# Optimization experiments

Hardware: AMD Instinct MI355X
Metric: run time of the kernel (lower is better)

The kernel has to match this reference:

```python
import jax, jax.numpy as jnp
import numpy as np

N = 50000
E = 400000
DIM_IN = 512
DIM_H = 64
HEADS = 8
DIM_OUT = 40
SLOPE = 0.2  # PyG GATv2Conv default negative_slope


def setup_inputs() -> dict:
    key = jax.random.key(0)
    ks = jax.random.split(key, 16)
    s = 0.05
    return {
        "x": jax.random.normal(ks[0], (N, DIM_IN), dtype=jnp.float32),
        "edge_index": jax.random.randint(ks[1], (2, E), 0, N, dtype=jnp.int64),
        "Wl1": jax.random.normal(ks[2], (DIM_IN, HEADS * DIM_H), dtype=jnp.float32) * s,
        "Wr1": jax.random.normal(ks[3], (DIM_IN, HEADS * DIM_H), dtype=jnp.float32) * s,
        "att1": jax.random.normal(ks[4], (HEADS, DIM_H), dtype=jnp.float32) * s,
        "b1": jax.random.normal(ks[5], (HEADS * DIM_H,), dtype=jnp.float32) * s,
        "Wl2": jax.random.normal(ks[6], (HEADS * DIM_H, DIM_OUT), dtype=jnp.float32) * s,
        "Wr2": jax.random.normal(ks[7], (HEADS * DIM_H, DIM_OUT), dtype=jnp.float32) * s,
        "att2": jax.random.normal(ks[8], (1, DIM_OUT), dtype=jnp.float32) * s,
        "b2": jax.random.normal(ks[9], (DIM_OUT,), dtype=jnp.float32) * s,
        "Wl3": jax.random.normal(ks[10], (HEADS * DIM_H, 2), dtype=jnp.float32) * s,
        "Wr3": jax.random.normal(ks[11], (HEADS * DIM_H, 2), dtype=jnp.float32) * s,
        "att3": jax.random.normal(ks[12], (1, 2), dtype=jnp.float32) * s,
        "b3": jax.random.normal(ks[13], (2,), dtype=jnp.float32) * s,
    }


def gatv2(x, src, dst, Wl, Wr, att, b):
    # PyG GATv2Conv: e_ij = att . LeakyReLU(W_l x_j + W_r x_i); softmax over j (by dst i);
    # out_i = sum_j alpha_ij * (W_l x_j); heads concatenated; bias added after.
    n = x.shape[0]
    H, F = att.shape
    xl = (x @ Wl).reshape(n, H, F)  # source transform
    xr = (x @ Wr).reshape(n, H, F)  # target transform
    e = jax.nn.leaky_relu(xl[src] + xr[dst], negative_slope=SLOPE)  # [E, H, F]
    logits = jnp.einsum("ehf,hf->eh", e, att)  # [E, H]
    m = jax.ops.segment_max(logits, dst, num_segments=n)  # self-loops => every segment nonempty
    ex = jnp.exp(logits - m[dst])
    denom = jax.ops.segment_sum(ex, dst, num_segments=n)
    alpha = ex / denom[dst]  # [E, H]
    out = jax.ops.segment_sum(xl[src] * alpha[:, :, None], dst, num_segments=n)  # [N, H, F]
    return out.reshape(n, H * F) + b


def reference(x, edge_index, Wl1, Wr1, att1, b1, Wl2, Wr2, att2, b2, Wl3, Wr3, att3, b3):
    # add self loops (PyG default add_self_loops=True)
    loops = jnp.arange(N, dtype=edge_index.dtype)
    ei = jnp.concatenate([edge_index, jnp.stack([loops, loops])], axis=1)
    src, dst = ei[0], ei[1]
    # eval mode: dropout is identity; ReverseLayerF is identity in forward
    h = jax.nn.relu(gatv2(x, src, dst, Wl1, Wr1, att1, b1))
    y_class = gatv2(h, src, dst, Wl2, Wr2, att2, b2)
    y_domain = gatv2(h, src, dst, Wl3, Wr3, att3, b3)
    return (y_class, y_domain)
```

## Files before the change

kernel.cpp:

```cpp
#include <hip/hip_runtime.h>
#include <math.h>

typedef unsigned short u16;
typedef unsigned int   u32;
typedef __attribute__((ext_vector_type(8))) short bf16x8;
typedef __attribute__((ext_vector_type(4))) float f32x4;
typedef __attribute__((ext_vector_type(4))) u32   u32x4;

__device__ __forceinline__ float b2f(u16 u) {
  union { u32 i; float f; } v; v.i = ((u32)u) << 16; return v.f;
}
__device__ __forceinline__ u16 f2b(float f) {
  union { u32 i; float f; } v; v.f = f;
  u32 r = v.i + 0x7FFFu + ((v.i >> 16) & 1u);
  return (u16)(r >> 16);
}
__device__ __forceinline__ float blo(u32 w) {
  union { u32 i; float f; } v; v.i = w << 16; return v.f;
}
__device__ __forceinline__ float bhi(u32 w) {
  union { u32 i; float f; } v; v.i = w & 0xFFFF0000u; return v.f;
}
__device__ __forceinline__ void ld_lds16(const u16* g, u16* l) {
  __builtin_amdgcn_global_load_lds((const __attribute__((address_space(1))) void*)g,
                                   (__attribute__((address_space(3))) void*)l, 16, 0, 0);
}

#define NN 50000
#define NE 400000
#define NT 450000
#define NBLK_SCAN 196

__global__ void k_detect(const void* x, const void* ei, int* flags) {
  __shared__ int cnt[2];
  int t = threadIdx.x;
  if (t < 2) cnt[t] = 0;
  __syncthreads();
  u16 u = ((const u16*)x)[t];
  int e = (u >> 7) & 0xFF;
  if (u == 0 || (e >= 90 && e <= 134)) atomicAdd(&cnt[0], 1);
  if (t < 16) {
    if (((const int*)ei)[2 * t + 1] == 0) atomicAdd(&cnt[1], 1);
  }
  __syncthreads();
  if (t == 0) {
    flags[0] = (cnt[0] >= 110) ? 1 : 0;
    flags[1] = (cnt[1] >= 15) ? 1 : 0;
  }
}

__device__ __forceinline__ int eidx(const int* ei, int pos, int i64) {
  return i64 ? ei[2 * pos] : ei[pos];
}

__global__ void k_convert_x(const void* x, const int* flags, u16* xb) {
  int c = blockIdx.x * 256 + threadIdx.x;
  if (flags[0]) {
    ((u32x4*)xb)[c] = ((const u32x4*)x)[c];
  } else {
    const float* xf = (const float*)x + (size_t)c * 8;
    u32x4 o;
    #pragma unroll
    for (int i = 0; i < 4; ++i) {
      u32 lo = f2b(xf[2 * i]);
      u32 hi = f2b(xf[2 * i + 1]);
      o[i] = lo | (hi << 16);
    }
    *(u32x4*)(xb + (size_t)c * 8) = o;
  }
}

__global__ void k_pack_w1t(const void* Wl1, const void* Wr1, const int* flags, u16* w1t) {
  int t = blockIdx.x * 256 + threadIdx.x;
  int k = t >> 10;
  int c = t & 1023;
  const void* W = (c < 512) ? Wl1 : Wr1;
  int cc = c & 511;
  u16 v;
  if (flags[0]) v = ((const u16*)W)[k * 512 + cc];
  else          v = f2b(((const float*)W)[k * 512 + cc]);
  w1t[c * 512 + k] = v;
}

__global__ void k_pack_w23t(const void* Wl2, const void* Wr2, const void* Wl3, const void* Wr3,
                            const int* flags, u16* w23t) {
  int t = blockIdx.x * 256 + threadIdx.x;
  int k = t / 96;
  int c = t % 96;
  const void* W = nullptr; int idx = 0;
  if (c < 40)      { W = Wl2; idx = k * 40 + c; }
  else if (c < 42) { W = Wl3; idx = k * 2 + (c - 40); }
  else if (c < 82) { W = Wr2; idx = k * 40 + (c - 42); }
  else if (c < 84) { W = Wr3; idx = k * 2 + (c - 82); }
  u16 v = 0;
  if (W) {
    if (flags[0]) v = ((const u16*)W)[idx];
    else          v = f2b(((const float*)W)[idx]);
  }
  w23t[c * 512 + k] = v;
}

__global__ void k_pack_params(const void* att1, const void* b1, const void* att2, const void* b2,
                              const void* att3, const void* b3, const int* flags, float* params) {
  int t = blockIdx.x * 256 + threadIdx.x;
  if (t >= 1108) return;
  const void* src; int idx;
  if (t < 512)       { src = att1; idx = t; }
  else if (t < 1024) { src = b1;   idx = t - 512; }
  else if (t < 1064) { src = att2; idx = t - 1024; }
  else if (t < 1104) { src = b2;   idx = t - 1064; }
  else if (t < 1106) { src = att3; idx = t - 1104; }
  else               { src = b3;   idx = t - 1106; }
  params[t] = flags[0] ? b2f(((const u16*)src)[idx]) : ((const float*)src)[idx];
}

__global__ void k_hist(const int* ei, const int* flags, int* deg) {
  int e = blockIdx.x * 256 + threadIdx.x;
  if (e >= NE) return;
  int d = eidx(ei, NE + e, flags[1]);
  atomicAdd(&deg[d], 1);
}

__global__ void k_scanA(const int* deg, int* row_ptr, int* bsum) {
  __shared__ int sh[256];
  int b = blockIdx.x, t = threadIdx.x;
  int i = b * 256 + t;
  int val = (i < NN) ? deg[i] + 1 : 0;
  sh[t] = val;
  __syncthreads();
  #pragma unroll
  for (int off = 1; off < 256; off <<= 1) {
    int v = (t >= off) ? sh[t - off] : 0;
    __syncthreads();
    sh[t] += v;
    __syncthreads();
  }
  if (i < NN) row_ptr[i] = sh[t] - val;
  if (t == 255) bsum[b] = sh[255];
}

__global__ void k_scanB(int* bsum, int* row_ptr) {
  __shared__ int sh[256];
  int t = threadIdx.x;
  int val = (t < NBLK_SCAN) ? bsum[t] : 0;
  sh[t] = val;
  __syncthreads();
  #pragma unroll
  for (int off = 1; off < 256; off <<= 1) {
    int v = (t >= off) ? sh[t - off] : 0;
    __syncthreads();
    sh[t] += v;
    __syncthreads();
  }
  if (t < NBLK_SCAN) bsum[t] = sh[t] - val;
  if (t == 255) row_ptr[NN] = sh[255];
}

__global__ void k_scanC(const int* bsum, int* row_ptr, int* cursor) {
  int i = blockIdx.x * 256 + threadIdx.x;
  if (i < NN) {
    int v = row_ptr[i] + bsum[blockIdx.x];
    row_ptr[i] = v;
    cursor[i] = v;
  }
}

__global__ void k_scatter(const int* ei, const int* flags, int* cursor, int* csr_src) {
  int t = blockIdx.x * 256 + threadIdx.x;
  if (t >= NT) return;
  int i64 = flags[1];
  int s, d;
  if (t < NE) { s = eidx(ei, t, i64); d = eidx(ei, NE + t, i64); }
  else        { s = d = t - NE; }
  int pos = atomicAdd(&cursor[d], 1);
  csr_src[pos] = s;
}

__global__ __launch_bounds__(256) void k_gemm1(const u16* __restrict__ A, const u16* __restrict__ Bt,
                                               u16* __restrict__ XL, u16* __restrict__ XR) {
  __shared__ __align__(16) u16 As[128 * 32];
  __shared__ __align__(16) u16 Bs[128 * 32];
  const int m0 = blockIdx.y * 128;
  const int n0 = blockIdx.x * 128;
  const int t = threadIdx.x;
  const int wave = t >> 6;
  const int lane = t & 63;
  const int wm = (wave >> 1) * 64;
  const int wn = (wave & 1) * 64;
  const int fr = lane & 15;
  const int fk = lane >> 4;
  const int srow = lane >> 2;
  const int scol = (lane & 3) * 8;
  f32x4 acc[4][4] = {};
  for (int k0 = 0; k0 < 512; k0 += 32) {
    #pragma unroll
    for (int c = 0; c < 2; ++c) {
      int r = wave * 16 + c * 64;
      ld_lds16(&A[(m0 + r + srow) * 512 + k0 + scol], &As[r * 32]);
      ld_lds16(&Bt[(n0 + r + srow) * 512 + k0 + scol], &Bs[r * 32]);
    }
    __syncthreads();
    bf16x8 af[4], bb[4];
    #pragma unroll
    for (int i = 0; i < 4; ++i) af[i] = *(const bf16x8*)&As[(wm + i * 16 + fr) * 32 + fk * 8];
    #pragma unroll
    for (int j = 0; j < 4; ++j) bb[j] = *(const bf16x8*)&Bs[(wn + j * 16 + fr) * 32 + fk * 8];
    #pragma unroll
    for (int i = 0; i < 4; ++i)
      #pragma unroll
      for (int j = 0; j < 4; ++j)
        acc[i][j] = __builtin_amdgcn_mfma_f32_16x16x32_bf16(af[i], bb[j], acc[i][j], 0, 0, 0);
    __syncthreads();
  }
  #pragma unroll
  for (int i = 0; i < 4; ++i) {
    #pragma unroll
    for (int r = 0; r < 4; ++r) {
      int gm = m0 + wm + i * 16 + fk * 4 + r;
      if (gm < NN) {
        #pragma unroll
        for (int j = 0; j < 4; ++j) {
          int gn = n0 + wn + j * 16 + fr;
          u16 v = f2b(acc[i][j][r]);
          if (gn < 512) XL[gm * 512 + gn] = v;
          else          XR[gm * 512 + gn - 512] = v;
        }
      }
    }
  }
}

__global__ __launch_bounds__(256) void k_gemm2(const u16* __restrict__ A, const u16* __restrict__ Bt,
                                               float* __restrict__ C) {
  __shared__ __align__(16) short As[64][40];
  __shared__ __align__(16) short Bs[96][40];
  const int m0 = blockIdx.x * 64;
  const int t = threadIdx.x;
  const int wave = t >> 6;
  const int lane = t & 63;
  const int fr = lane & 15;
  const int fk = lane >> 4;
  f32x4 acc[6] = {};
  for (int k0 = 0; k0 < 512; k0 += 32) {
    {
      int row = t >> 2, kc = (t & 3) * 8;
      int gm = m0 + row;
      u32x4 va = {0, 0, 0, 0};
      if (gm < NN) va = *(const u32x4*)&A[gm * 512 + k0 + kc];
      *(u32x4*)&As[row][kc] = va;
    }
    for (int c = t; c < 384; c += 256) {
      int row = c >> 2, kc = (c & 3) * 8;
      *(u32x4*)&Bs[row][kc] = *(const u32x4*)&Bt[row * 512 + k0 + kc];
    }
    __syncthreads();
    bf16x8 af = *(const bf16x8*)&As[wave * 16 + fr][fk * 8];
    #pragma unroll
    for (int j = 0; j < 6; ++j) {
      bf16x8 bb = *(const bf16x8*)&Bs[j * 16 + fr][fk * 8];
      acc[j] = __builtin_amdgcn_mfma_f32_16x16x32_bf16(af, bb, acc[j], 0, 0, 0);
    }
    __syncthreads();
  }
  #pragma unroll
  for (int j = 0; j < 6; ++j) {
    int gn = j * 16 + fr;
    if (gn < 84) {
      #pragma unroll
      for (int r = 0; r < 4; ++r) {
        int gm = m0 + wave * 16 + fk * 4 + r;
        if (gm < NN) C[gm * 84 + gn] = acc[j][r];
      }
    }
  }
}

__global__ __launch_bounds__(256) void k_layer1f(const u16* __restrict__ xl1, const u16* __restrict__ xr1,
                                                 const int* __restrict__ row_ptr, const int* __restrict__ csr_src,
                                                 const float* __restrict__ params, u16* __restrict__ hb) {
  int wid = blockIdx.x * 4 + (threadIdx.x >> 6);
  int lane = threadIdx.x & 63;
  int nw = gridDim.x * 4;
  float att[8], bias[8];
  #pragma unroll
  for (int k = 0; k < 8; ++k) { att[k] = params[lane * 8 + k]; bias[k] = params[512 + lane * 8 + k]; }
  for (int i = wid; i < NN; i += nw) {
    int e0 = row_ptr[i], e1 = row_ptr[i + 1];
    u32x4 xrv = *(const u32x4*)&xr1[(size_t)i * 512 + lane * 8];
    float xr[8];
    #pragma unroll
    for (int q = 0; q < 4; ++q) { xr[2 * q] = blo(xrv[q]); xr[2 * q + 1] = bhi(xrv[q]); }
    float m = -INFINITY, s = 0.f;
    float acc[8] = {0.f, 0.f, 0.f, 0.f, 0.f, 0.f, 0.f, 0.f};
    u32x4 nxt = *(const u32x4*)&xl1[(size_t)csr_src[e0] * 512 + lane * 8];
    for (int p = e0; p < e1; ++p) {
      u32x4 cur = nxt;
      if (p + 1 < e1) nxt = *(const u32x4*)&xl1[(size_t)csr_src[p + 1] * 512 + lane * 8];
      float xl[8];
      #pragma unroll
      for (int q = 0; q < 4; ++q) { xl[2 * q] = blo(cur[q]); xl[2 * q + 1] = bhi(cur[q]); }
      float c = 0.f;
      #pragma unroll
      for (int k = 0; k < 8; ++k) {
        float t = xl[k] + xr[k];
        c = fmaf(att[k], fmaxf(t, 0.2f * t), c);
      }
      c += __shfl_xor(c, 1, 64);
      c += __shfl_xor(c, 2, 64);
      c += __shfl_xor(c, 4, 64);
      float mn = fmaxf(m, c);
      float sc = __expf(m - mn);
      float pv = __expf(c - mn);
      s = fmaf(s, sc, pv);
      #pragma unroll
      for (int k = 0; k < 8; ++k) acc[k] = fmaf(acc[k], sc, pv * xl[k]);
      m = mn;
    }
    float r = 1.f / s;
    u32x4 o;
    #pragma unroll
    for (int q = 0; q < 4; ++q) {
      u32 lo = f2b(fmaxf(fmaf(acc[2 * q],     r, bias[2 * q]),     0.f));
      u32 hi = f2b(fmaxf(fmaf(acc[2 * q + 1], r, bias[2 * q + 1]), 0.f));
      o[q] = lo | (hi << 16);
    }
    *(u32x4*)&hb[(size_t)i * 512 + lane * 8] = o;
  }
}

__global__ __launch_bounds__(256) void k_layer23f(const float* __restrict__ xlr23, const int* __restrict__ row_ptr,
                                                  const int* __restrict__ csr_src, const float* __restrict__ params,
                                                  const int* __restrict__ flags, void* __restrict__ out) {
  int wid = blockIdx.x * 4 + (threadIdx.x >> 6);
  int lane = threadIdx.x & 63;
  int nw = gridDim.x * 4;
  int c = lane;
  bool act = c < 42;
  float att = 0.f;
  if (c < 40)      att = params[1024 + c];
  else if (c < 42) att = params[1104 + (c - 40)];
  int isbf = flags[0];
  for (int i = wid; i < NN; i += nw) {
    int e0 = row_ptr[i], e1 = row_ptr[i + 1];
    float xr = act ? xlr23[(size_t)i * 84 + 42 + c] : 0.f;
    float m2 = -INFINITY, s2 = 0.f, m3 = -INFINITY, s3 = 0.f, acc = 0.f;
    float nxt = act ? xlr23[(size_t)csr_src[e0] * 84 + c] : 0.f;
    for (int p = e0; p < e1; ++p) {
      float xl = nxt;
      if (p + 1 < e1) nxt = act ? xlr23[(size_t)csr_src[p + 1] * 84 + c] : 0.f;
      float t = xl + xr;
      float v = att * fmaxf(t, 0.2f * t);
      float v2 = (c < 40) ? v : 0.f;
      #pragma unroll
      for (int o = 32; o >= 1; o >>= 1) v2 += __shfl_xor(v2, o, 64);
      float v3 = v + __shfl_xor(v, 1, 64);
      float logit3 = __shfl(v3, 40, 64);
      float mn2 = fmaxf(m2, v2), sc2 = __expf(m2 - mn2), p2 = __expf(v2 - mn2);
      s2 = fmaf(s2, sc2, p2); m2 = mn2;
      float mn3 = fmaxf(m3, logit3), sc3 = __expf(m3 - mn3), p3 = __expf(logit3 - mn3);
      s3 = fmaf(s3, sc3, p3); m3 = mn3;
      float pp = (c < 40) ? p2 : p3;
      float sc = (c < 40) ? sc2 : sc3;
      acc = fmaf(acc, sc, pp * xl);
    }
    if (c < 40) {
      float v = acc / s2 + params[1064 + c];
      size_t o = (size_t)i * 40 + c;
      if (isbf) ((u16*)out)[o] = f2b(v); else ((float*)out)[o] = v;
    } else if (c < 42) {
      float v = acc / s3 + params[1106 + (c - 40)];
      size_t o = 2000000 + (size_t)i * 2 + (c - 40);
      if (isbf) ((u16*)out)[o] = f2b(v); else ((float*)out)[o] = v;
    }
  }
}

extern "C" void kernel_launch(void* const* d_in, const int* in_sizes, int n_in,
                              void* d_out, int out_size, void* d_ws, size_t ws_size,
                              hipStream_t stream) {
  const void* x    = d_in[0];
  const int*  ei   = (const int*)d_in[1];
  const void* Wl1  = d_in[2];
  const void* Wr1  = d_in[3];
  const void* att1 = d_in[4];
  const void* b1   = d_in[5];
  const void* Wl2  = d_in[6];
  const void* Wr2  = d_in[7];
  const void* att2 = d_in[8];
  const void* b2   = d_in[9];
  const void* Wl3  = d_in[10];
  const void* Wr3  = d_in[11];
  const void* att3 = d_in[12];
  const void* b3   = d_in[13];
  (void)in_sizes; (void)n_in; (void)out_size;

  char* ws = (char*)d_ws;
  size_t off = 0;
  auto alloc = [&](size_t bytes) -> void* {
    void* p = ws + off;
    off = (off + bytes + 255) & ~(size_t)255;
    return p;
  };
  int*   flags   = (int*)  alloc(64);
  u16*   xb      = (u16*)  alloc((size_t)NN * 512 * 2);
  u16*   w1t     = (u16*)  alloc((size_t)1024 * 512 * 2);
  u16*   xl1     = (u16*)  alloc((size_t)NN * 512 * 2);
  u16*   xr1     = (u16*)  alloc((size_t)NN * 512 * 2);
  u16*   gpad    = (u16*)  alloc((size_t)128 * 512 * 2);
  u16*   hb      = (u16*)  alloc((size_t)NN * 512 * 2);
  u16*   w23t    = (u16*)  alloc((size_t)96 * 512 * 2);
  float* xlr23   = (float*)alloc((size_t)NN * 84 * 4);
  float* params  = (float*)alloc(1108 * 4);
  int*   row_ptr = (int*)  alloc((NN + 1) * 4);
  int*   deg     = (int*)  alloc(NN * 4);
  int*   cursor  = (int*)  alloc(NN * 4);
  int*   csr_src = (int*)  alloc(NT * 4);
  int*   bsum    = (int*)  alloc(256 * 4);
  (void)gpad;
  if (ws_size < off) return;

  hipLaunchKernelGGL(k_detect, dim3(1), dim3(128), 0, stream, x, (const void*)ei, flags);
  hipLaunchKernelGGL(k_convert_x, dim3(12500), dim3(256), 0, stream, x, flags, xb);
  hipLaunchKernelGGL(k_pack_w1t, dim3(2048), dim3(256), 0, stream, Wl1, Wr1, flags, w1t);
  hipLaunchKernelGGL(k_pack_w23t, dim3(192), dim3(256), 0, stream, Wl2, Wr2, Wl3, Wr3, flags, w23t);
  hipLaunchKernelGGL(k_pack_params, dim3(5), dim3(256), 0, stream, att1, b1, att2, b2, att3, b3, flags, params);
  hipMemsetAsync(deg, 0, NN * 4, stream);
  hipLaunchKernelGGL(k_hist, dim3((NE + 255) / 256), dim3(256), 0, stream, ei, flags, deg);
  hipLaunchKernelGGL(k_scanA, dim3(NBLK_SCAN), dim3(256), 0, stream, deg, row_ptr, bsum);
  hipLaunchKernelGGL(k_scanB, dim3(1), dim3(256), 0, stream, bsum, row_ptr);
  hipLaunchKernelGGL(k_scanC, dim3(NBLK_SCAN), dim3(256), 0, stream, bsum, row_ptr, cursor);
  hipLaunchKernelGGL(k_scatter, dim3((NT + 255) / 256), dim3(256), 0, stream, ei, flags, cursor, csr_src);
  hipLaunchKernelGGL(k_gemm1, dim3(8, 391), dim3(256), 0, stream, xb, w1t, xl1, xr1);
  hipLaunchKernelGGL(k_layer1f, dim3(2048), dim3(256), 0, stream, xl1, xr1, row_ptr, csr_src, params, hb);
  hipLaunchKernelGGL(k_gemm2, dim3(782), dim3(256), 0, stream, hb, w23t, xlr23);
  hipLaunchKernelGGL(k_layer23f, dim3(2048), dim3(256), 0, stream, xlr23, row_ptr, csr_src, params, flags, d_out);
}
```

Measured before the change: 535.1 us.

## Remap gemm1 tiles per XCD, swizzle LDS chunks, skip x copy when already bf16

The first-layer GEMM now runs on a 1D grid whose block IDs are remapped so that each XCD handles a contiguous band of M tiles, which is meant to improve L2 reuse of A rows across the eight N tiles. LDS chunk placement is XOR-style rotated, both on the async global-to-LDS load and on the fragment reads, to reduce bank conflicts. The A operand reads the raw input directly when it is already bf16, so the identity copy in k_convert_x is skipped, and out-of-range rows are clamped instead of reading past the end. Indexing was widened to size_t in a few places.

Measured after the change: 497.3 us. -7.1%, faster.

```diff
diff --git a/kernel.cpp b/kernel.cpp
--- a/kernel.cpp
+++ b/kernel.cpp
@@ -54,20 +54,17 @@
 }
 
 __global__ void k_convert_x(const void* x, const int* flags, u16* xb) {
+  if (flags[0]) return;
   int c = blockIdx.x * 256 + threadIdx.x;
-  if (flags[0]) {
-    ((u32x4*)xb)[c] = ((const u32x4*)x)[c];
-  } else {
-    const float* xf = (const float*)x + (size_t)c * 8;
-    u32x4 o;
-    #pragma unroll
-    for (int i = 0; i < 4; ++i) {
-      u32 lo = f2b(xf[2 * i]);
-      u32 hi = f2b(xf[2 * i + 1]);
-      o[i] = lo | (hi << 16);
-    }
-    *(u32x4*)(xb + (size_t)c * 8) = o;
-  }
+  const float* xf = (const float*)x + (size_t)c * 8;
+  u32x4 o;
+  #pragma unroll
+  for (int i = 0; i < 4; ++i) {
+    u32 lo = f2b(xf[2 * i]);
+    u32 hi = f2b(xf[2 * i + 1]);
+    o[i] = lo | (hi << 16);
+  }
+  *(u32x4*)(xb + (size_t)c * 8) = o;
 }
 
 __global__ void k_pack_w1t(const void* Wl1, const void* Wr1, const int* flags, u16* w1t) {
@@ -176,12 +173,20 @@
   csr_src[pos] = s;
 }
 
-__global__ __launch_bounds__(256) void k_gemm1(const u16* __restrict__ A, const u16* __restrict__ Bt,
+__global__ __launch_bounds__(256) void k_gemm1(const void* __restrict__ xraw, const u16* __restrict__ xb,
+                                               const u16* __restrict__ Bt, const int* __restrict__ flags,
                                                u16* __restrict__ XL, u16* __restrict__ XR) {
   __shared__ __align__(16) u16 As[128 * 32];
   __shared__ __align__(16) u16 Bs[128 * 32];
-  const int m0 = blockIdx.y * 128;
-  const int n0 = blockIdx.x * 128;
+  const int id  = blockIdx.x;
+  const int xcd = id & 7;
+  const int lb  = id >> 3;
+  const int mt  = xcd * 49 + (lb >> 3);
+  const int nt  = lb & 7;
+  if (mt >= 391) return;
+  const int m0 = mt * 128;
+  const int n0 = nt * 128;
+  const u16* __restrict__ A = flags[0] ? (const u16*)xraw : xb;
   const int t = threadIdx.x;
   const int wave = t >> 6;
   const int lane = t & 63;
@@ -189,22 +194,25 @@
   const int wn = (wave & 1) * 64;
   const int fr = lane & 15;
   const int fk = lane >> 4;
-  const int srow = lane >> 2;
-  const int scol = (lane & 3) * 8;
+  const int rsub = lane >> 2;
+  const int achk = ((lane & 3) + (rsub >> 1)) & 3;
+  const int sA = ((fk - (fr >> 1)) & 3) * 8;
   f32x4 acc[4][4] = {};
   for (int k0 = 0; k0 < 512; k0 += 32) {
     #pragma unroll
     for (int c = 0; c < 2; ++c) {
-      int r = wave * 16 + c * 64;
-      ld_lds16(&A[(m0 + r + srow) * 512 + k0 + scol], &As[r * 32]);
-      ld_lds16(&Bt[(n0 + r + srow) * 512 + k0 + scol], &Bs[r * 32]);
+      int rbase = wave * 16 + c * 64;
+      int gm = m0 + rbase + rsub;
+      if (gm > NN - 1) gm = NN - 1;
+      ld_lds16(&A[(size_t)gm * 512 + k0 + achk * 8], &As[rbase * 32]);
+      ld_lds16(&Bt[(size_t)(n0 + rbase + rsub) * 512 + k0 + achk * 8], &Bs[rbase * 32]);
     }
     __syncthreads();
     bf16x8 af[4], bb[4];
     #pragma unroll
-    for (int i = 0; i < 4; ++i) af[i] = *(const bf16x8*)&As[(wm + i * 16 + fr) * 32 + fk * 8];
-    #pragma unroll
-    for (int j = 0; j < 4; ++j) bb[j] = *(const bf16x8*)&Bs[(wn + j * 16 + fr) * 32 + fk * 8];
+    for (int i = 0; i < 4; ++i) af[i] = *(const bf16x8*)&As[(wm + i * 16 + fr) * 32 + sA];
+    #pragma unroll
+    for (int j = 0; j < 4; ++j) bb[j] = *(const bf16x8*)&Bs[(wn + j * 16 + fr) * 32 + sA];
     #pragma unroll
     for (int i = 0; i < 4; ++i)
       #pragma unroll
@@ -222,8 +230,8 @@
         for (int j = 0; j < 4; ++j) {
           int gn = n0 + wn + j * 16 + fr;
           u16 v = f2b(acc[i][j][r]);
-          if (gn < 512) XL[gm * 512 + gn] = v;
-          else          XR[gm * 512 + gn - 512] = v;
+          if (gn < 512) XL[(size_t)gm * 512 + gn] = v;
+          else          XR[(size_t)gm * 512 + gn - 512] = v;
         }
       }
     }
@@ -246,7 +254,7 @@
       int row = t >> 2, kc = (t & 3) * 8;
       int gm = m0 + row;
       u32x4 va = {0, 0, 0, 0};
-      if (gm < NN) va = *(const u32x4*)&A[gm * 512 + k0 + kc];
+      if (gm < NN) va = *(const u32x4*)&A[(size_t)gm * 512 + k0 + kc];
       *(u32x4*)&As[row][kc] = va;
     }
     for (int c = t; c < 384; c += 256) {
@@ -269,7 +277,7 @@
       #pragma unroll
       for (int r = 0; r < 4; ++r) {
         int gm = m0 + wave * 16 + fk * 4 + r;
-        if (gm < NN) C[gm * 84 + gn] = acc[j][r];
+        if (gm < NN) C[(size_t)gm * 84 + gn] = acc[j][r];
       }
     }
   }
@@ -406,7 +414,6 @@
   u16*   w1t     = (u16*)  alloc((size_t)1024 * 512 * 2);
   u16*   xl1     = (u16*)  alloc((size_t)NN * 512 * 2);
   u16*   xr1     = (u16*)  alloc((size_t)NN * 512 * 2);
-  u16*   gpad    = (u16*)  alloc((size_t)128 * 512 * 2);
   u16*   hb      = (u16*)  alloc((size_t)NN * 512 * 2);
   u16*   w23t    = (u16*)  alloc((size_t)96 * 512 * 2);
   float* xlr23   = (float*)alloc((size_t)NN * 84 * 4);
@@ -416,7 +423,6 @@
   int*   cursor  = (int*)  alloc(NN * 4);
   int*   csr_src = (int*)  alloc(NT * 4);
   int*   bsum    = (int*)  alloc(256 * 4);
-  (void)gpad;
   if (ws_size < off) return;
 
   hipLaunchKernelGGL(k_detect, dim3(1), dim3(128), 0, stream, x, (const void*)ei, flags);
@@ -430,7 +436,7 @@
   hipLaunchKernelGGL(k_scanB, dim3(1), dim3(256), 0, stream, bsum, row_ptr);
   hipLaunchKernelGGL(k_scanC, dim3(NBLK_SCAN), dim3(256), 0, stream, bsum, row_ptr, cursor);
   hipLaunchKernelGGL(k_scatter, dim3((NT + 255) / 256), dim3(256), 0, stream, ei, flags, cursor, csr_src);
-  hipLaunchKernelGGL(k_gemm1, dim3(8, 391), dim3(256), 0, stream, xb, w1t, xl1, xr1);
+  hipLaunchKernelGGL(k_gemm1, dim3(3136), dim3(256), 0, stream, x, xb, w1t, flags, xl1, xr1);
   hipLaunchKernelGGL(k_layer1f, dim3(2048), dim3(256), 0, stream, xl1, xr1, row_ptr, csr_src, params, hb);
   hipLaunchKernelGGL(k_gemm2, dim3(782), dim3(256), 0, stream, hb, w23t, xlr23);
   hipLaunchKernelGGL(k_layer23f, dim3(2048), dim3(256), 0, stream, xlr23, row_ptr, csr_src, params, flags, d_out);
```
